# Kernel tuning notes

Hardware: AMD Instinct MI355X
Metric: run time of the kernel (lower is better)

The kernel has to match this reference:

```python
import jax, jax.numpy as jnp
import numpy as np

N = 50000      # nodes
E = 1600000    # message edges (avg degree 32)
EQ = 500000    # link-prediction query edges
IN, HID, OUT, FCH = 128, 128, 64, 256
ALPHA = 0.5


def setup_inputs() -> dict:
    key = jax.random.key(0)
    ks = jax.random.split(key, 8)
    def p(k, shape):
        fan_in = shape[0]
        return jax.random.normal(k, shape, jnp.float32) * (1.0 / np.sqrt(fan_in))
    return {
        "x": jax.random.normal(ks[0], (N, IN), jnp.float32),
        "edge_index": jax.random.randint(ks[1], (2, E), 0, N),
        "edge_label_index": jax.random.randint(ks[2], (2, EQ), 0, N),
        "W1": p(ks[3], (IN, HID)),  "b1": jnp.zeros((HID,), jnp.float32),
        "W2": p(ks[4], (HID, OUT)), "b2": jnp.zeros((OUT,), jnp.float32),
        "Wf1": p(ks[5], (IN, FCH)), "bf1": jnp.zeros((FCH,), jnp.float32),
        "Wf2": p(ks[6], (FCH, OUT)), "bf2": jnp.zeros((OUT,), jnp.float32),
    }


def reference(x, edge_index, edge_label_index, W1, b1, W2, b2, Wf1, bf1, Wf2, bf2):
    n = x.shape[0]
    # GCN self-loops + symmetric normalization (PyG GCNConv defaults)
    loop = jnp.arange(n)
    src = jnp.concatenate([edge_index[0], loop])
    dst = jnp.concatenate([edge_index[1], loop])
    deg = jax.ops.segment_sum(jnp.ones_like(dst, jnp.float32), dst, num_segments=n)
    dinv = jnp.where(deg > 0, jax.lax.rsqrt(deg), 0.0)
    norm = dinv[src] * dinv[dst]  # [E+N]

    def gcn(h, W, b):
        h = h @ W                                  # transform first (PyG order)
        msg = norm[:, None] * h[src]               # gather + scale per edge
        return jax.ops.segment_sum(msg, dst, num_segments=n) + b

    x_gcn = jax.nn.relu(gcn(x, W1, b1))
    x_gcn = gcn(x_gcn, W2, b2)
    x_fc = jax.nn.relu(x @ Wf1 + bf1) @ Wf2 + bf2
    z = x_gcn * (1.0 - ALPHA) + x_fc * ALPHA       # [N, OUT]
    # edge dot-product decode
    return jnp.sum(z[edge_label_index[0]] * z[edge_label_index[1]], axis=1)
```

## Files before the change

kernel.cpp:

```cpp
#include <hip/hip_runtime.h>

#define FIN   128
#define FHID  128
#define FOUT  64
#define FFC   256
#define CHUNK 4096
#define BKBITS 7
#define BKN   128
#define ECAP  4608

typedef __attribute__((ext_vector_type(8))) short          bf16x8;
typedef __attribute__((ext_vector_type(4))) float          f32x4;
typedef __attribute__((ext_vector_type(2))) float          f32x2;
typedef __attribute__((ext_vector_type(8))) unsigned short u16x8;

static __device__ __forceinline__ unsigned short f2bf(float f) {
    unsigned int u = __float_as_uint(f);
    u = (u + 0x7fffu + ((u >> 16) & 1u)) >> 16;
    return (unsigned short)u;
}
static __device__ __forceinline__ float bf2f(unsigned short s) {
    return __uint_as_float(((unsigned int)s) << 16);
}
static __device__ __forceinline__ void accum_fp8(float* acc, uint4 g) {
    f32x2 p;
    p = __builtin_amdgcn_cvt_pk_f32_fp8(g.x, false); acc[0]  += p.x; acc[1]  += p.y;
    p = __builtin_amdgcn_cvt_pk_f32_fp8(g.x, true);  acc[2]  += p.x; acc[3]  += p.y;
    p = __builtin_amdgcn_cvt_pk_f32_fp8(g.y, false); acc[4]  += p.x; acc[5]  += p.y;
    p = __builtin_amdgcn_cvt_pk_f32_fp8(g.y, true);  acc[6]  += p.x; acc[7]  += p.y;
    p = __builtin_amdgcn_cvt_pk_f32_fp8(g.z, false); acc[8]  += p.x; acc[9]  += p.y;
    p = __builtin_amdgcn_cvt_pk_f32_fp8(g.z, true);  acc[10] += p.x; acc[11] += p.y;
    p = __builtin_amdgcn_cvt_pk_f32_fp8(g.w, false); acc[12] += p.x; acc[13] += p.y;
    p = __builtin_amdgcn_cvt_pk_f32_fp8(g.w, true);  acc[14] += p.x; acc[15] += p.y;
}

__global__ __launch_bounds__(256) void binA_cvt_kernel(
    const int* __restrict__ src, const int* __restrict__ dst,
    int* __restrict__ bcur, unsigned int* __restrict__ ebuf, int E, int NBA,
    const float* __restrict__ W1, const float* __restrict__ W2,
    const float* __restrict__ Wf1, const float* __restrict__ Wf2,
    unsigned short* __restrict__ w1t, unsigned short* __restrict__ w2t,
    unsigned short* __restrict__ wf1t, unsigned short* __restrict__ wf2t)
{
    int t = threadIdx.x;
    if (blockIdx.x >= NBA) {
        long i = (long)(blockIdx.x - NBA) * 256 + t;
        if (i < 16384) {
            int k = (int)i >> 7, n = (int)i & 127;
            w1t[n * 128 + k] = f2bf(W1[i]);
        } else if (i < 24576) {
            int j = (int)i - 16384; int k = j >> 6, n = j & 63;
            w2t[n * 128 + k] = f2bf(W2[j]);
        } else if (i < 57344) {
            int j = (int)i - 24576; int k = j >> 8, n = j & 255;
            wf1t[n * 128 + k] = f2bf(Wf1[j]);
        } else if (i < 73728) {
            int j = (int)i - 57344; int k = j >> 6, n = j & 63;
            wf2t[n * 256 + k] = f2bf(Wf2[j]);
        }
        return;
    }
    __shared__ int hist[512];
    __shared__ int rstart[512];
    __shared__ int lcur[512];
    hist[t] = 0; hist[t + 256] = 0; lcur[t] = 0; lcur[t + 256] = 0;
    __syncthreads();
    int e0 = blockIdx.x * CHUNK;
    int e1 = min(e0 + CHUNK, E);
    for (int e = e0 + t; e < e1; e += 256)
        atomicAdd(&hist[dst[e] >> BKBITS], 1);
    __syncthreads();
    if (hist[t])       rstart[t]       = atomicAdd(&bcur[t],       hist[t]);
    if (hist[t + 256]) rstart[t + 256] = atomicAdd(&bcur[t + 256], hist[t + 256]);
    __syncthreads();
    for (int e = e0 + t; e < e1; e += 256) {
        int s = src[e], d = dst[e];
        int b = d >> BKBITS;
        int pos = rstart[b] + atomicAdd(&lcur[b], 1);
        if (pos < ECAP)
            ebuf[(size_t)b * ECAP + pos] =
                ((unsigned)s << BKBITS) | ((unsigned)d & (BKN - 1));
    }
}

__global__ __launch_bounds__(256) void binB_fc_kernel(
    const unsigned int* __restrict__ ebuf, const int* __restrict__ bcnt,
    int2* __restrict__ rp2, int* __restrict__ col, float* __restrict__ dinv,
    unsigned char* __restrict__ xs, int N, int NBK,
    const float* __restrict__ X,
    const unsigned short* __restrict__ B1T,
    const unsigned short* __restrict__ B2T,
    const float* __restrict__ bias1, const float* __restrict__ bias2,
    float* __restrict__ C, int M)
{
    __shared__ __align__(16) unsigned char smem[65536];
    const int tid = threadIdx.x;

    if (blockIdx.x < NBK) {
        int* cnt           = (int*)smem;
        int* tmp           = (int*)(smem + 512);
        int* ccur          = (int*)(smem + 1536);
        int* scur          = (int*)(smem + 2048);
        float* sdinv       = (float*)(smem + 3072);
        unsigned int* skey = (unsigned int*)(smem + 3584);
        int b = blockIdx.x;
        int t = tid;
        size_t base = (size_t)b * ECAP;
        int ne = min(bcnt[b], ECAP);
        if (t < 128) cnt[t] = 0;
        scur[t] = 0;
        __syncthreads();
        for (int e = t; e < ne; e += 256) {
            unsigned int k = ebuf[base + e];
            atomicAdd(&cnt[k & (BKN - 1)], 1);
            atomicAdd(&scur[k >> 15], 1);
        }
        __syncthreads();
        int c = (t < 128) ? cnt[t] : 0;
        tmp[t] = c;
        __syncthreads();
        int acc = c;
        for (int off = 1; off < 128; off <<= 1) {
            int a = (t >= off) ? tmp[t - off] : 0;
            __syncthreads();
            acc += a; tmp[t] = acc;
            __syncthreads();
        }
        if (t < 128) {
            float di = rsqrtf((float)c + 1.0f);
            sdinv[t] = di;
            int node = b * BKN + t;
            int st = (int)base + acc - c;
            if (node < N) { dinv[node] = di; rp2[node] = make_int2(st, st + c); }
            ccur[t] = st;
        }
        __syncthreads();
        int sv = scur[t];
        tmp[t] = sv;
        __syncthreads();
        int sacc = sv;
        for (int off = 1; off < 256; off <<= 1) {
            int a = (t >= off) ? tmp[t - off] : 0;
            __syncthreads();
            sacc += a; tmp[t] = sacc;
            __syncthreads();
        }
        scur[t] = sacc - sv;
        __syncthreads();
        for (int e = t; e < ne; e += 256) {
            unsigned int k = ebuf[base + e];
            int pos = atomicAdd(&scur[k >> 15], 1);
            skey[pos] = k;
        }
        __syncthreads();
        for (int w = 0; w < ne; w += 256) {
            int e = w + t;
            if (e < ne) {
                unsigned int k = skey[e];
                int pos = atomicAdd(&ccur[k & (BKN - 1)], 1);
                col[pos] = (int)(k >> BKBITS);
            }
            __syncthreads();
        }
        int nl0 = t >> 3;
        int f0 = (t & 7) << 4;
        #pragma unroll
        for (int it = 0; it < 4; it++) {
            int nl = it * 32 + nl0;
            int gn = b * BKN + nl;
            if (gn >= N) continue;
            float d2 = sdinv[nl];
            const float* xr = X + (size_t)gn * FIN + f0;
            float4 va = *(const float4*)(xr);
            float4 vb = *(const float4*)(xr + 4);
            float4 vc = *(const float4*)(xr + 8);
            float4 vd = *(const float4*)(xr + 12);
            float f[16] = { va.x * d2, va.y * d2, va.z * d2, va.w * d2,
                            vb.x * d2, vb.y * d2, vb.z * d2, vb.w * d2,
                            vc.x * d2, vc.y * d2, vc.z * d2, vc.w * d2,
                            vd.x * d2, vd.y * d2, vd.z * d2, vd.w * d2 };
            uint4 w;
            w.x = 0; w.y = 0; w.z = 0; w.w = 0;
            w.x = __builtin_amdgcn_cvt_pk_fp8_f32(f[0],  f[1],  w.x, false);
            w.x = __builtin_amdgcn_cvt_pk_fp8_f32(f[2],  f[3],  w.x, true);
            w.y = __builtin_amdgcn_cvt_pk_fp8_f32(f[4],  f[5],  w.y, false);
            w.y = __builtin_amdgcn_cvt_pk_fp8_f32(f[6],  f[7],  w.y, true);
            w.z = __builtin_amdgcn_cvt_pk_fp8_f32(f[8],  f[9],  w.z, false);
            w.z = __builtin_amdgcn_cvt_pk_fp8_f32(f[10], f[11], w.z, true);
            w.w = __builtin_amdgcn_cvt_pk_fp8_f32(f[12], f[13], w.w, false);
            w.w = __builtin_amdgcn_cvt_pk_fp8_f32(f[14], f[15], w.w, true);
            *(uint4*)(xs + (size_t)gn * 128 + f0) = w;
        }
        return;
    }

    unsigned short* lds = (unsigned short*)smem;
    const int lane = tid & 63;
    const int wave = tid >> 6;
    const int m = lane & 15;
    const int q = lane >> 4;
    const int rowbase = (blockIdx.x - NBK) * 64 + wave * 16;
    const int row = rowbase + m;

    float4 av[8] = {};
    {
        const float* arow = X + (size_t)row * FIN + q * 8;
        if (row < M) {
            #pragma unroll
            for (int kk = 0; kk < 4; kk++) {
                av[2 * kk]     = *(const float4*)(arow + kk * 32);
                av[2 * kk + 1] = *(const float4*)(arow + kk * 32 + 4);
            }
        }
    }

    #pragma unroll 4
    for (int i = tid; i < 4096; i += 256) {
        int n = i >> 4, sl = i & 15;
        ((u16x8*)lds)[(n << 4) | (sl ^ (n & 7))] = ((const u16x8*)B1T)[i];
    }
    __syncthreads();

    f32x4 acc[16] = {};
    for (int k0 = 0; k0 < 128; k0 += 32) {
        int kk = k0 >> 5;
        float4 a0 = av[2 * kk], a1 = av[2 * kk + 1];
        bf16x8 a;
        a[0] = (short)f2bf(a0.x); a[1] = (short)f2bf(a0.y);
        a[2] = (short)f2bf(a0.z); a[3] = (short)f2bf(a0.w);
        a[4] = (short)f2bf(a1.x); a[5] = (short)f2bf(a1.y);
        a[6] = (short)f2bf(a1.z); a[7] = (short)f2bf(a1.w);
        int sl = q + (k0 >> 3);
        #pragma unroll
        for (int c = 0; c < 16; c++) {
            int cc = c * 16 + m;
            bf16x8 b = ((const bf16x8*)lds)[(cc << 4) | (sl ^ (cc & 7))];
            acc[c] = __builtin_amdgcn_mfma_f32_16x16x32_bf16(a, b, acc[c], 0, 0, 0);
        }
    }
    __syncthreads();

    #pragma unroll 2
    for (int i = tid; i < 2048; i += 256) {
        int n = i >> 5, sl = i & 31;
        ((u16x8*)lds)[2048 + ((n << 5) | (sl ^ (n & 7)))] = ((const u16x8*)B2T)[i];
    }
    #pragma unroll
    for (int c = 0; c < 16; c++) {
        int cc = c * 16 + m;
        float bv = bias1[cc];
        #pragma unroll
        for (int r = 0; r < 4; r++) {
            int rr = wave * 16 + q * 4 + r;
            float v = fmaxf(acc[c][r] + bv, 0.f);
            lds[rr * 256 + ((((cc >> 3) ^ (rr & 7)) << 3) | (cc & 7))] = f2bf(v);
        }
    }
    __syncthreads();

    f32x4 acc2[4] = {};
    {
        int rr = wave * 16 + m;
        for (int k0 = 0; k0 < 256; k0 += 32) {
            int sl = q + (k0 >> 3);
            bf16x8 a = ((const bf16x8*)lds)[(rr << 5) | (sl ^ (rr & 7))];
            #pragma unroll
            for (int c = 0; c < 4; c++) {
                int cc = c * 16 + m;
                bf16x8 b = ((const bf16x8*)lds)[2048 + ((cc << 5) | (sl ^ (cc & 7)))];
                acc2[c] = __builtin_amdgcn_mfma_f32_16x16x32_bf16(a, b, acc2[c], 0, 0, 0);
            }
        }
    }
    __syncthreads();

    constexpr int ROWB = 4 * 16 * 4 + 16;
    unsigned char* wbase = (unsigned char*)lds + wave * 16 * ROWB;
    #pragma unroll
    for (int c = 0; c < 4; c++) {
        int lc = c * 16 + m;
        float bv = bias2[lc];
        #pragma unroll
        for (int r = 0; r < 4; r++)
            ((float*)(wbase + (q * 4 + r) * ROWB))[lc] = acc2[c][r] + bv;
    }
    #pragma unroll
    for (int p = 0; p < 4; p++) {
        int r2 = p * 4 + (lane >> 4);
        int bo = (lane & 15) * 16;
        int gr = rowbase + r2;
        if (gr < M) {
            uint4 v = *(const uint4*)(wbase + r2 * ROWB + bo);
            *(uint4*)((unsigned char*)C + (size_t)gr * FOUT * 4 + bo) = v;
        }
    }
}

__global__ __launch_bounds__(256) void pull1_kernel(
    const unsigned char* __restrict__ xs, const int2* __restrict__ rp2,
    const int* __restrict__ col, const float* __restrict__ dinv,
    unsigned short* __restrict__ aggx, int N)
{
    int tid = threadIdx.x;
    int node = blockIdx.x * 32 + (tid >> 3);
    if (node >= N) return;
    int f0 = (tid & 7) << 4;
    const unsigned char* base = xs + f0;
    float di = dinv[node];
    int2 se = rp2[node];
    float acc[16] = {};
    accum_fp8(acc, *(const uint4*)(base + (size_t)node * 128));
    int e = se.x, end = se.y;
    for (; e + 4 <= end; e += 4) {
        int s0 = col[e], s1 = col[e + 1], s2 = col[e + 2], s3 = col[e + 3];
        uint4 g0 = *(const uint4*)(base + (size_t)s0 * 128);
        uint4 g1 = *(const uint4*)(base + (size_t)s1 * 128);
        uint4 g2 = *(const uint4*)(base + (size_t)s2 * 128);
        uint4 g3 = *(const uint4*)(base + (size_t)s3 * 128);
        accum_fp8(acc, g0); accum_fp8(acc, g1);
        accum_fp8(acc, g2); accum_fp8(acc, g3);
    }
    for (; e < end; e++)
        accum_fp8(acc, *(const uint4*)(base + (size_t)col[e] * 128));
    u16x8 o0, o1;
    #pragma unroll
    for (int j = 0; j < 8; j++) {
        o0[j] = f2bf(di * acc[j]);
        o1[j] = f2bf(di * acc[8 + j]);
    }
    *(u16x8*)(aggx + (size_t)node * FIN + f0)     = o0;
    *(u16x8*)(aggx + (size_t)node * FIN + f0 + 8) = o1;
}

__global__ __launch_bounds__(256) void gcn_kernel(
    const unsigned short* __restrict__ A,
    const unsigned short* __restrict__ B1T,
    const unsigned short* __restrict__ B2T,
    const float* __restrict__ bias1,
    const float* __restrict__ rowscale,
    unsigned short* __restrict__ C, int M)
{
    __shared__ __align__(16) unsigned short lds[24576];
    const int tid  = threadIdx.x;
    const int lane = tid & 63;
    const int wave = tid >> 6;
    const int m = lane & 15;
    const int q = lane >> 4;
    const int rowbase = blockIdx.x * 64 + wave * 16;
    const int row = rowbase + m;

    bf16x8 areg[4] = {};
    {
        const unsigned short* arow = A + (size_t)row * FIN + q * 8;
        if (row < M) {
            #pragma unroll
            for (int kk = 0; kk < 4; kk++)
                areg[kk] = *(const bf16x8*)(arow + kk * 32);
        }
    }

    #pragma unroll 2
    for (int i = tid; i < 2048; i += 256) {
        int n = i >> 4, sl = i & 15;
        ((u16x8*)lds)[(n << 4) | (sl ^ (n & 7))] = ((const u16x8*)B1T)[i];
    }
    #pragma unroll 2
    for (int i = tid; i < 1024; i += 256) {
        int n = i >> 4, sl = i & 15;
        ((u16x8*)lds)[2048 + ((n << 4) | (sl ^ (n & 7)))] = ((const u16x8*)B2T)[i];
    }
    __syncthreads();

    f32x4 acc[8] = {};
    for (int k0 = 0; k0 < 128; k0 += 32) {
        bf16x8 a = areg[k0 >> 5];
        int sl = q + (k0 >> 3);
        #pragma unroll
        for (int c = 0; c < 8; c++) {
            int cc = c * 16 + m;
            bf16x8 b = ((const bf16x8*)lds)[(cc << 4) | (sl ^ (cc & 7))];
            acc[c] = __builtin_amdgcn_mfma_f32_16x16x32_bf16(a, b, acc[c], 0, 0, 0);
        }
    }
    __syncthreads();

    #pragma unroll
    for (int c = 0; c < 8; c++) {
        int cc = c * 16 + m;
        float bv = bias1[cc];
        #pragma unroll
        for (int r = 0; r < 4; r++) {
            int rr = wave * 16 + q * 4 + r;
            float v = fmaxf(acc[c][r] + bv, 0.f);
            lds[rr * 128 + ((((cc >> 3) ^ (rr & 7)) << 3) | (cc & 7))] = f2bf(v);
        }
    }
    __syncthreads();

    f32x4 acc2[4] = {};
    {
        int rr = wave * 16 + m;
        for (int k0 = 0; k0 < 128; k0 += 32) {
            int sl = q + (k0 >> 3);
            bf16x8 a = ((const bf16x8*)lds)[(rr << 4) | (sl ^ (rr & 7))];
            #pragma unroll
            for (int c = 0; c < 4; c++) {
                int cc = c * 16 + m;
                bf16x8 b = ((const bf16x8*)lds)[2048 + ((cc << 4) | (sl ^ (cc & 7)))];
                acc2[c] = __builtin_amdgcn_mfma_f32_16x16x32_bf16(a, b, acc2[c], 0, 0, 0);
            }
        }
    }
    float rs[4];
    #pragma unroll
    for (int r = 0; r < 4; r++) {
        int gr = rowbase + q * 4 + r;
        rs[r] = (gr < M) ? rowscale[gr] : 1.0f;
    }
    __syncthreads();

    constexpr int ROWB = 4 * 16 * 2 + 16;
    unsigned char* wbase = (unsigned char*)lds + wave * 16 * ROWB;
    #pragma unroll
    for (int c = 0; c < 4; c++) {
        int lc = c * 16 + m;
        #pragma unroll
        for (int r = 0; r < 4; r++)
            ((unsigned short*)(wbase + (q * 4 + r) * ROWB))[lc] =
                f2bf(acc2[c][r] * rs[r]);
    }
    #pragma unroll
    for (int p = 0; p < 2; p++) {
        int r2 = p * 8 + (lane >> 3);
        int bo = (lane & 7) * 16;
        int gr = rowbase + r2;
        if (gr < M) {
            uint4 v = *(const uint4*)(wbase + r2 * ROWB + bo);
            *(uint4*)((unsigned char*)C + (size_t)gr * FOUT * 2 + bo) = v;
        }
    }
}

__global__ __launch_bounds__(256) void pull2_kernel(
    const unsigned short* __restrict__ t2s, const int2* __restrict__ rp2,
    const int* __restrict__ col, const float* __restrict__ dinv,
    const float* __restrict__ xfc, const float* __restrict__ b2,
    unsigned short* __restrict__ zbf, int N)
{
    int tid = threadIdx.x;
    int node = blockIdx.x * 32 + (tid >> 3);
    if (node >= N) return;
    int f0 = (tid & 7) << 3;
    const unsigned short* base = t2s + f0;
    float di = dinv[node];
    float4 x0 = *(const float4*)(xfc + (size_t)node * FOUT + f0);
    float4 x1 = *(const float4*)(xfc + (size_t)node * FOUT + f0 + 4);
    float4 bb0 = *(const float4*)(b2 + f0);
    float4 bb1 = *(const float4*)(b2 + f0 + 4);
    u16x8 own = *(const u16x8*)(base + (size_t)node * FOUT);
    float acc[8];
    #pragma unroll
    for (int j = 0; j < 8; j++) acc[j] = bf2f(own[j]);
    int2 se = rp2[node];
    int e = se.x, end = se.y;
    for (; e + 4 <= end; e += 4) {
        int s0 = col[e], s1 = col[e + 1], s2 = col[e + 2], s3 = col[e + 3];
        u16x8 v0 = *(const u16x8*)(base + (size_t)s0 * FOUT);
        u16x8 v1 = *(const u16x8*)(base + (size_t)s1 * FOUT);
        u16x8 v2 = *(const u16x8*)(base + (size_t)s2 * FOUT);
        u16x8 v3 = *(const u16x8*)(base + (size_t)s3 * FOUT);
        #pragma unroll
        for (int j = 0; j < 8; j++)
            acc[j] += (bf2f(v0[j]) + bf2f(v1[j])) + (bf2f(v2[j]) + bf2f(v3[j]));
    }
    for (; e < end; e++) {
        u16x8 v = *(const u16x8*)(base + (size_t)col[e] * FOUT);
        #pragma unroll
        for (int j = 0; j < 8; j++) acc[j] += bf2f(v[j]);
    }
    float xf[8] = { x0.x, x0.y, x0.z, x0.w, x1.x, x1.y, x1.z, x1.w };
    float bv[8] = { bb0.x, bb0.y, bb0.z, bb0.w, bb1.x, bb1.y, bb1.z, bb1.w };
    u16x8 o;
    #pragma unroll
    for (int j = 0; j < 8; j++)
        o[j] = f2bf(0.5f * (di * acc[j] + bv[j]) + 0.5f * xf[j]);
    *(u16x8*)(zbf + (size_t)node * FOUT + f0) = o;
}

__global__ void decode_kernel(
    const unsigned short* __restrict__ zbf, const int* __restrict__ eli,
    float* __restrict__ out, int Q)
{
    int tid = blockIdx.x * blockDim.x + threadIdx.x;
    int q = tid >> 3;
    if (q >= Q) return;
    int lane = tid & 7;
    int a = eli[q];
    int b = eli[Q + q];
    u16x8 va = *(const u16x8*)(zbf + (size_t)a * FOUT + lane * 8);
    u16x8 vb = *(const u16x8*)(zbf + (size_t)b * FOUT + lane * 8);
    float s = 0.f;
    #pragma unroll
    for (int j = 0; j < 8; j++) s += bf2f(va[j]) * bf2f(vb[j]);
    s += __shfl_down(s, 4, 8);
    s += __shfl_down(s, 2, 8);
    s += __shfl_down(s, 1, 8);
    if (lane == 0) out[q] = s;
}

extern "C" void kernel_launch(void* const* d_in, const int* in_sizes, int n_in,
                              void* d_out, int out_size, void* d_ws, size_t ws_size,
                              hipStream_t stream)
{
    const float* x   = (const float*)d_in[0];
    const int*   ei  = (const int*)  d_in[1];
    const int*   eli = (const int*)  d_in[2];
    const float* W1  = (const float*)d_in[3];
    const float* b1  = (const float*)d_in[4];
    const float* W2  = (const float*)d_in[5];
    const float* b2  = (const float*)d_in[6];
    const float* Wf1 = (const float*)d_in[7];
    const float* bf1 = (const float*)d_in[8];
    const float* Wf2 = (const float*)d_in[9];
    const float* bf2 = (const float*)d_in[10];
    float* out = (float*)d_out;

    const int N = in_sizes[0] / FIN;
    const int E = in_sizes[1] / 2;
    const int Q = in_sizes[2] / 2;
    const int* src = ei;
    const int* dst = ei + E;
    const int NBK = (N + BKN - 1) >> BKBITS;
    const int NBA = (E + CHUNK - 1) / CHUNK;
    const int NCV = 73728 / 256;
    const int NFC = (N + 63) / 64;

    char* p = (char*)d_ws;
    float* dinv = (float*)p;             p += (size_t)N * 4;
    int2*  rp2  = (int2*)p;              p += (size_t)N * 8;
    int*   bcur = (int*)p;               p += 2048;
    unsigned short* w1t  = (unsigned short*)p; p += FIN * FHID * 2;
    unsigned short* w2t  = (unsigned short*)p; p += FHID * FOUT * 2;
    unsigned short* wf1t = (unsigned short*)p; p += FIN * FFC * 2;
    unsigned short* wf2t = (unsigned short*)p; p += FFC * FOUT * 2;
    float* xfc = (float*)p;              p += (size_t)N * FOUT * 4;
    unsigned char* xs = (unsigned char*)p;     p += (size_t)N * 128;
    unsigned int* ebuf = (unsigned int*)p;  p += (size_t)NBK * ECAP * 4;
    int*   col  = (int*)p;               p += (size_t)NBK * ECAP * 4;
    unsigned short* aggx = (unsigned short*)p; p += (size_t)N * FIN * 2;
    unsigned short* t2s  = (unsigned short*)p; p += (size_t)N * FOUT * 2;
    unsigned short* zbf  = (unsigned short*)p; p += (size_t)N * FOUT * 2;

    const int TB = 256;

    hipMemsetAsync(bcur, 0, 2048, stream);

    binA_cvt_kernel<<<NBA + NCV, TB, 0, stream>>>(
        src, dst, bcur, ebuf, E, NBA,
        W1, W2, Wf1, Wf2, w1t, w2t, wf1t, wf2t);

    binB_fc_kernel<<<NBK + NFC, TB, 0, stream>>>(
        ebuf, bcur, rp2, col, dinv, xs, N, NBK,
        x, wf1t, wf2t, bf1, bf2, xfc, N);

    pull1_kernel<<<(N + 31) / 32, TB, 0, stream>>>(xs, rp2, col, dinv, aggx, N);

    gcn_kernel<<<(N + 63) / 64, TB, 0, stream>>>(
        aggx, w1t, w2t, b1, dinv, t2s, N);

    pull2_kernel<<<(N + 31) / 32, TB, 0, stream>>>(
        t2s, rp2, col, dinv, xfc, b2, zbf, N);

    {
        long total = (long)Q * 8;
        decode_kernel<<<(int)((total + TB - 1) / TB), TB, 0, stream>>>(
            zbf, eli, out, Q);
    }
}
```

Measured before the change: 246.2 us.

## Shrink LDS in FC and GCN kernels by staging weights in halves; store xfc as bf16

The FC branch of binB_fc_kernel now loads Wf1 and Wf2 into shared memory in two halves, one after another, with extra barriers. This cuts its static LDS from 64KB to 48KB. gcn_kernel likewise loads W2 only after the first GEMM, reusing space and shrinking LDS from 48KB to 32KB. The intermediate xfc buffer is now written and read as bf16 instead of fp32, halving that traffic. The aim is higher occupancy and less memory traffic, at the cost of extra syncs, a serialized weight load and some precision loss in the FC output.

```diff
diff --git a/kernel.cpp b/kernel.cpp
--- a/kernel.cpp
+++ b/kernel.cpp
@@ -91,9 +91,9 @@
     const unsigned short* __restrict__ B1T,
     const unsigned short* __restrict__ B2T,
     const float* __restrict__ bias1, const float* __restrict__ bias2,
-    float* __restrict__ C, int M)
+    unsigned short* __restrict__ C, int M)
 {
-    __shared__ __align__(16) unsigned char smem[65536];
+    __shared__ __align__(16) unsigned char smem[49152];
     const int tid = threadIdx.x;
 
     if (blockIdx.x < NBK) {
@@ -214,8 +214,8 @@
         }
     }
 
-    #pragma unroll 4
-    for (int i = tid; i < 4096; i += 256) {
+    #pragma unroll 2
+    for (int i = tid; i < 2048; i += 256) {
         int n = i >> 4, sl = i & 15;
         ((u16x8*)lds)[(n << 4) | (sl ^ (n & 7))] = ((const u16x8*)B1T)[i];
     }
@@ -232,19 +232,36 @@
         a[6] = (short)f2bf(a1.z); a[7] = (short)f2bf(a1.w);
         int sl = q + (k0 >> 3);
         #pragma unroll
-        for (int c = 0; c < 16; c++) {
+        for (int c = 0; c < 8; c++) {
             int cc = c * 16 + m;
             bf16x8 b = ((const bf16x8*)lds)[(cc << 4) | (sl ^ (cc & 7))];
             acc[c] = __builtin_amdgcn_mfma_f32_16x16x32_bf16(a, b, acc[c], 0, 0, 0);
         }
     }
     __syncthreads();
-
     #pragma unroll 2
     for (int i = tid; i < 2048; i += 256) {
-        int n = i >> 5, sl = i & 31;
-        ((u16x8*)lds)[2048 + ((n << 5) | (sl ^ (n & 7)))] = ((const u16x8*)B2T)[i];
-    }
+        int n = i >> 4, sl = i & 15;
+        ((u16x8*)lds)[(n << 4) | (sl ^ (n & 7))] = ((const u16x8*)B1T)[2048 + i];
+    }
+    __syncthreads();
+    for (int k0 = 0; k0 < 128; k0 += 32) {
+        int kk = k0 >> 5;
+        float4 a0 = av[2 * kk], a1 = av[2 * kk + 1];
+        bf16x8 a;
+        a[0] = (short)f2bf(a0.x); a[1] = (short)f2bf(a0.y);
+        a[2] = (short)f2bf(a0.z); a[3] = (short)f2bf(a0.w);
+        a[4] = (short)f2bf(a1.x); a[5] = (short)f2bf(a1.y);
+        a[6] = (short)f2bf(a1.z); a[7] = (short)f2bf(a1.w);
+        int sl = q + (k0 >> 3);
+        #pragma unroll
+        for (int c = 0; c < 8; c++) {
+            int cc = c * 16 + m;
+            bf16x8 b = ((const bf16x8*)lds)[(cc << 4) | (sl ^ (cc & 7))];
+            acc[8 + c] = __builtin_amdgcn_mfma_f32_16x16x32_bf16(a, b, acc[8 + c], 0, 0, 0);
+        }
+    }
+    __syncthreads();
     #pragma unroll
     for (int c = 0; c < 16; c++) {
         int cc = c * 16 + m;
@@ -256,25 +273,51 @@
             lds[rr * 256 + ((((cc >> 3) ^ (rr & 7)) << 3) | (cc & 7))] = f2bf(v);
         }
     }
+    for (int i = tid; i < 1024; i += 256) {
+        int n = i >> 4, sl = i & 15;
+        ((u16x8*)lds)[2048 + ((n << 4) | (sl ^ (n & 7)))] =
+            ((const u16x8*)B2T)[n * 32 + sl];
+    }
     __syncthreads();
 
     f32x4 acc2[4] = {};
     {
         int rr = wave * 16 + m;
-        for (int k0 = 0; k0 < 256; k0 += 32) {
+        for (int k0 = 0; k0 < 128; k0 += 32) {
             int sl = q + (k0 >> 3);
             bf16x8 a = ((const bf16x8*)lds)[(rr << 5) | (sl ^ (rr & 7))];
             #pragma unroll
             for (int c = 0; c < 4; c++) {
                 int cc = c * 16 + m;
-                bf16x8 b = ((const bf16x8*)lds)[2048 + ((cc << 5) | (sl ^ (cc & 7)))];
+                bf16x8 b = ((const bf16x8*)lds)[2048 + ((cc << 4) | (sl ^ (cc & 7)))];
                 acc2[c] = __builtin_amdgcn_mfma_f32_16x16x32_bf16(a, b, acc2[c], 0, 0, 0);
             }
         }
     }
     __syncthreads();
-
-    constexpr int ROWB = 4 * 16 * 4 + 16;
+    for (int i = tid; i < 1024; i += 256) {
+        int n = i >> 4, sl = i & 15;
+        ((u16x8*)lds)[2048 + ((n << 4) | (sl ^ (n & 7)))] =
+            ((const u16x8*)B2T)[n * 32 + 16 + sl];
+    }
+    __syncthreads();
+    {
+        int rr = wave * 16 + m;
+        for (int k0 = 128; k0 < 256; k0 += 32) {
+            int sla = q + (k0 >> 3);
+            int slb = q + ((k0 - 128) >> 3);
+            bf16x8 a = ((const bf16x8*)lds)[(rr << 5) | (sla ^ (rr & 7))];
+            #pragma unroll
+            for (int c = 0; c < 4; c++) {
+                int cc = c * 16 + m;
+                bf16x8 b = ((const bf16x8*)lds)[2048 + ((cc << 4) | (slb ^ (cc & 7)))];
+                acc2[c] = __builtin_amdgcn_mfma_f32_16x16x32_bf16(a, b, acc2[c], 0, 0, 0);
+            }
+        }
+    }
+    __syncthreads();
+
+    constexpr int ROWB = 4 * 16 * 2 + 16;
     unsigned char* wbase = (unsigned char*)lds + wave * 16 * ROWB;
     #pragma unroll
     for (int c = 0; c < 4; c++) {
@@ -282,16 +325,17 @@
         float bv = bias2[lc];
         #pragma unroll
         for (int r = 0; r < 4; r++)
-            ((float*)(wbase + (q * 4 + r) * ROWB))[lc] = acc2[c][r] + bv;
-    }
-    #pragma unroll
-    for (int p = 0; p < 4; p++) {
-        int r2 = p * 4 + (lane >> 4);
-        int bo = (lane & 15) * 16;
+            ((unsigned short*)(wbase + (q * 4 + r) * ROWB))[lc] =
+                f2bf(acc2[c][r] + bv);
+    }
+    #pragma unroll
+    for (int p = 0; p < 2; p++) {
+        int r2 = p * 8 + (lane >> 3);
+        int bo = (lane & 7) * 16;
         int gr = rowbase + r2;
         if (gr < M) {
             uint4 v = *(const uint4*)(wbase + r2 * ROWB + bo);
-            *(uint4*)((unsigned char*)C + (size_t)gr * FOUT * 4 + bo) = v;
+            *(uint4*)((unsigned char*)C + (size_t)gr * FOUT * 2 + bo) = v;
         }
     }
 }
@@ -340,7 +384,7 @@
     const float* __restrict__ rowscale,
     unsigned short* __restrict__ C, int M)
 {
-    __shared__ __align__(16) unsigned short lds[24576];
+    __shared__ __align__(16) unsigned short lds[16384];
     const int tid  = threadIdx.x;
     const int lane = tid & 63;
     const int wave = tid >> 6;
@@ -364,11 +408,6 @@
         int n = i >> 4, sl = i & 15;
         ((u16x8*)lds)[(n << 4) | (sl ^ (n & 7))] = ((const u16x8*)B1T)[i];
     }
-    #pragma unroll 2
-    for (int i = tid; i < 1024; i += 256) {
-        int n = i >> 4, sl = i & 15;
-        ((u16x8*)lds)[2048 + ((n << 4) | (sl ^ (n & 7)))] = ((const u16x8*)B2T)[i];
-    }
     __syncthreads();
 
     f32x4 acc[8] = {};
@@ -394,6 +433,10 @@
             float v = fmaxf(acc[c][r] + bv, 0.f);
             lds[rr * 128 + ((((cc >> 3) ^ (rr & 7)) << 3) | (cc & 7))] = f2bf(v);
         }
+    }
+    for (int i = tid; i < 1024; i += 256) {
+        int n = i >> 4, sl = i & 15;
+        ((u16x8*)lds)[1024 + ((n << 4) | (sl ^ (n & 7)))] = ((const u16x8*)B2T)[i];
     }
     __syncthreads();
 
@@ -406,7 +449,7 @@
             #pragma unroll
             for (int c = 0; c < 4; c++) {
                 int cc = c * 16 + m;
-                bf16x8 b = ((const bf16x8*)lds)[2048 + ((cc << 4) | (sl ^ (cc & 7)))];
+                bf16x8 b = ((const bf16x8*)lds)[1024 + ((cc << 4) | (sl ^ (cc & 7)))];
                 acc2[c] = __builtin_amdgcn_mfma_f32_16x16x32_bf16(a, b, acc2[c], 0, 0, 0);
             }
         }
@@ -444,7 +487,7 @@
 __global__ __launch_bounds__(256) void pull2_kernel(
     const unsigned short* __restrict__ t2s, const int2* __restrict__ rp2,
     const int* __restrict__ col, const float* __restrict__ dinv,
-    const float* __restrict__ xfc, const float* __restrict__ b2,
+    const unsigned short* __restrict__ xfc, const float* __restrict__ b2,
     unsigned short* __restrict__ zbf, int N)
 {
     int tid = threadIdx.x;
@@ -453,8 +496,7 @@
     int f0 = (tid & 7) << 3;
     const unsigned short* base = t2s + f0;
     float di = dinv[node];
-    float4 x0 = *(const float4*)(xfc + (size_t)node * FOUT + f0);
-    float4 x1 = *(const float4*)(xfc + (size_t)node * FOUT + f0 + 4);
+    u16x8 xv = *(const u16x8*)(xfc + (size_t)node * FOUT + f0);
     float4 bb0 = *(const float4*)(b2 + f0);
     float4 bb1 = *(const float4*)(b2 + f0 + 4);
     u16x8 own = *(const u16x8*)(base + (size_t)node * FOUT);
@@ -478,12 +520,11 @@
         #pragma unroll
         for (int j = 0; j < 8; j++) acc[j] += bf2f(v[j]);
     }
-    float xf[8] = { x0.x, x0.y, x0.z, x0.w, x1.x, x1.y, x1.z, x1.w };
     float bv[8] = { bb0.x, bb0.y, bb0.z, bb0.w, bb1.x, bb1.y, bb1.z, bb1.w };
     u16x8 o;
     #pragma unroll
     for (int j = 0; j < 8; j++)
-        o[j] = f2bf(0.5f * (di * acc[j] + bv[j]) + 0.5f * xf[j]);
+        o[j] = f2bf(0.5f * (di * acc[j] + bv[j]) + 0.5f * bf2f(xv[j]));
     *(u16x8*)(zbf + (size_t)node * FOUT + f0) = o;
 }
 
@@ -543,7 +584,7 @@
     unsigned short* w2t  = (unsigned short*)p; p += FHID * FOUT * 2;
     unsigned short* wf1t = (unsigned short*)p; p += FIN * FFC * 2;
     unsigned short* wf2t = (unsigned short*)p; p += FFC * FOUT * 2;
-    float* xfc = (float*)p;              p += (size_t)N * FOUT * 4;
+    unsigned short* xfc = (unsigned short*)p;  p += (size_t)N * FOUT * 2;
     unsigned char* xs = (unsigned char*)p;     p += (size_t)N * 128;
     unsigned int* ebuf = (unsigned int*)p;  p += (size_t)NBK * ECAP * 4;
     int*   col  = (int*)p;               p += (size_t)NBK * ECAP * 4;
```

Result: no change. 243.0 us (-1.3%).
